# Performance work log

Measured on AMD Instinct MI355X. Metric: run time of the kernel, lower is better.

The kernel has to match this reference:

```python
import jax, jax.numpy as jnp
import numpy as np

V, E, H, L = 10000, 300, 256, 9   # vocab, embed_dim, hidden_dim, num_labels
B, T = 128, 512                   # batch, seq_len


def setup_inputs() -> dict:
    key = jax.random.key(0)
    ks = jax.random.split(key, 14)
    s = 0.05
    emb = jax.random.normal(ks[2], (V, E), jnp.float32) * s
    emb = emb.at[0].set(0.0)  # padding_idx=0
    return {
        "input_ids": jax.random.randint(ks[0], (B, T), 0, V),
        "attention_mask": jnp.ones((B, T), jnp.int32),
        "labels": jax.random.randint(ks[1], (B, T), 0, L),
        "emb": emb,
        "Wih_f": jax.random.normal(ks[3], (4 * H, E), jnp.float32) * s,
        "Whh_f": jax.random.normal(ks[4], (4 * H, H), jnp.float32) * s,
        "b_f": jnp.zeros((4 * H,), jnp.float32),
        "Wih_b": jax.random.normal(ks[5], (4 * H, E), jnp.float32) * s,
        "Whh_b": jax.random.normal(ks[6], (4 * H, H), jnp.float32) * s,
        "b_b": jnp.zeros((4 * H,), jnp.float32),
        "Wc": jax.random.normal(ks[7], (L, 2 * H), jnp.float32) * s,
        "bc": jnp.zeros((L,), jnp.float32),
        "transitions": jax.random.normal(ks[8], (L, L), jnp.float32) * 0.1,
        "start_trans": jax.random.normal(ks[9], (L,), jnp.float32) * 0.1,
        "end_trans": jax.random.normal(ks[10], (L,), jnp.float32) * 0.1,
    }


def _lstm_dir(x, Wih, Whh, b):
    # x: (T, B, E) -> hidden states (T, B, H); PyTorch gate order i,f,g,o
    Bn = x.shape[1]
    h0 = jnp.zeros((Bn, Whh.shape[1]), x.dtype)
    c0 = jnp.zeros((Bn, Whh.shape[1]), x.dtype)
    # precompute input projections once (big GEMM), scan only does small HxH GEMM
    xp = jnp.einsum('tbe,ge->tbg', x, Wih) + b
    def step(carry, xg):
        h, c = carry
        g = xg + h @ Whh.T
        i, f, gg, o = jnp.split(g, 4, axis=-1)
        c = jax.nn.sigmoid(f) * c + jax.nn.sigmoid(i) * jnp.tanh(gg)
        h = jax.nn.sigmoid(o) * jnp.tanh(c)
        return (h, c), h
    _, hs = jax.lax.scan(step, (h0, c0), xp)
    return hs


def reference(input_ids, attention_mask, labels, emb, Wih_f, Whh_f, b_f,
              Wih_b, Whh_b, b_b, Wc, bc, transitions, start_trans, end_trans):
    x = emb[input_ids]                       # (B, T, E)
    xt = jnp.transpose(x, (1, 0, 2))         # (T, B, E)
    hf = _lstm_dir(xt, Wih_f, Whh_f, b_f)
    hb = _lstm_dir(xt[::-1], Wih_b, Whh_b, b_b)[::-1]
    h = jnp.concatenate([hf, hb], axis=-1)   # (T, B, 2H); dropout is identity in eval
    em = h @ Wc.T + bc                       # (T, B, L) emissions

    mask = jnp.transpose(attention_mask, (1, 0)).astype(bool)  # (T, B)
    tags = jnp.transpose(labels, (1, 0))                        # (T, B)
    Bn = em.shape[1]
    bidx = jnp.arange(Bn)

    # --- numerator: score of gold path (torchcrf._compute_score) ---
    score0 = start_trans[tags[0]] + em[0, bidx, tags[0]]
    def num_step(carry, inp):
        score, prev = carry
        e_t, t_t, m_t = inp
        score = score + (transitions[prev, t_t] + e_t[bidx, t_t]) * m_t
        return (score, t_t), None
    (score, _), _ = jax.lax.scan(
        num_step, (score0, tags[0]),
        (em[1:], tags[1:], mask[1:].astype(em.dtype)))
    seq_ends = mask.astype(jnp.int32).sum(0) - 1
    last_tags = tags[seq_ends, bidx]
    score = score + end_trans[last_tags]

    # --- denominator: log partition (torchcrf._compute_normalizer) ---
    alpha0 = start_trans + em[0]             # (B, L)
    def den_step(alpha, inp):
        e_t, m_t = inp
        nxt = jax.nn.logsumexp(alpha[:, :, None] + transitions[None] + e_t[:, None, :], axis=1)
        return jnp.where(m_t[:, None], nxt, alpha), None
    alpha, _ = jax.lax.scan(den_step, alpha0, (em[1:], mask[1:]))
    logZ = jax.nn.logsumexp(alpha + end_trans, axis=-1)

    llh = score - logZ
    return -jnp.mean(llh)  # crf(..., reduction='mean'), negated
```

## Files before the change

kernel.cpp:

```cpp
#include <hip/hip_runtime.h>
#include <hip/hip_bf16.h>
#include <hip/hip_fp16.h>

#define Vn 10000
#define En 300
#define E2n 150
#define Hn 256
#define Gn 1024
#define Ln 9
#define Bn 128
#define Tn 512

#if defined(__has_builtin)
#  if __has_builtin(__builtin_amdgcn_sdot8)
#    define HAS_SDOT8 1
#  endif
#  if __has_builtin(__builtin_amdgcn_fdot2)
#    define HAS_FDOT2 1
#  endif
#endif
#ifndef HAS_SDOT8
#  define HAS_SDOT8 0
#endif
#ifndef HAS_FDOT2
#  define HAS_FDOT2 0
#endif

typedef _Float16 half2_t __attribute__((ext_vector_type(2)));

static __device__ __forceinline__ float bf2f(unsigned short u) {
    return __uint_as_float(((unsigned int)u) << 16);
}
static __device__ __forceinline__ unsigned short f2bf(float f) {
    unsigned int x = __float_as_uint(f);
    return (unsigned short)((x + 0x7FFFu + ((x >> 16) & 1u)) >> 16);
}
static __device__ __forceinline__ float sigm(float x) {
    return 1.f / (1.f + __expf(-x));
}
static __device__ __forceinline__ float tanh_fast(float x) {
    return 2.f / (1.f + __expf(-2.f * x)) - 1.f;
}
static __device__ __forceinline__ int dot8(unsigned int w, int h, int acc) {
#if HAS_SDOT8
    return __builtin_amdgcn_sdot8((int)w, h, acc, false);
#else
    unsigned int wl = ((w & 0x0F0F0F0Fu) ^ 0x08080808u) - 0x08080808u;
    unsigned int wh = (((w >> 4) & 0x0F0F0F0Fu) ^ 0x08080808u) - 0x08080808u;
    unsigned int hl = (((unsigned)h & 0x0F0F0F0Fu) ^ 0x08080808u) - 0x08080808u;
    unsigned int hh = ((((unsigned)h >> 4) & 0x0F0F0F0Fu) ^ 0x08080808u) - 0x08080808u;
    acc = __builtin_amdgcn_sdot4((int)wl, (int)hl, acc, false);
    return __builtin_amdgcn_sdot4((int)wh, (int)hh, acc, false);
#endif
}
static __device__ __forceinline__ float fdot2f(unsigned int a, unsigned int b, float acc) {
#if HAS_FDOT2
    return __builtin_amdgcn_fdot2(__builtin_bit_cast(half2_t, a),
                                  __builtin_bit_cast(half2_t, b), acc, false);
#else
    half2_t av = __builtin_bit_cast(half2_t, a);
    half2_t bv = __builtin_bit_cast(half2_t, b);
    return acc + (float)av.x * (float)bv.x + (float)av.y * (float)bv.y;
#endif
}
static __device__ __forceinline__ unsigned int packf16(float a, float b) {
    half2_t v = {(_Float16)a, (_Float16)b};
    return __builtin_bit_cast(unsigned int, v);
}

__global__ __launch_bounds__(256) void k_prep_emb(
    const float* __restrict__ emb, unsigned int* __restrict__ embp) {
    int n = blockIdx.x * 256 + threadIdx.x;
    if (n >= Vn * E2n) return;
    int v = n / E2n, e2 = n % E2n;
    float a = emb[(size_t)v * En + 2 * e2];
    float b = emb[(size_t)v * En + 2 * e2 + 1];
    embp[n] = packf16(a, b);
}

__global__ __launch_bounds__(256) void k_prep_wt(
    const float* __restrict__ Wf, const float* __restrict__ Wb,
    unsigned int* __restrict__ Tf, unsigned int* __restrict__ Tb) {
    int n = blockIdx.x * 256 + threadIdx.x;
    const float* src = blockIdx.y ? Wb : Wf;
    unsigned int* dst = blockIdx.y ? Tb : Tf;
    int e2 = n / Gn, j = n % Gn;
    float a = src[(size_t)j * En + 2 * e2];
    float b = src[(size_t)j * En + 2 * e2 + 1];
    dst[n] = packf16(a, b);
}

__global__ __launch_bounds__(64) void k_quant_whh(
    const float* __restrict__ Wf, const float* __restrict__ Wb,
    unsigned int* __restrict__ qr_f, unsigned int* __restrict__ ql_f,
    unsigned int* __restrict__ qr_b, unsigned int* __restrict__ ql_b,
    float* __restrict__ scl_f, float* __restrict__ scl_b) {
    int j = blockIdx.x;
    int dir = blockIdx.y;
    int lane = threadIdx.x;
    const float* W = dir ? Wb : Wf;
    float w8[8];
    float m = 0.f;
    if (lane < 32) {
        float4 wlo = *(const float4*)&W[(size_t)j * Hn + 8 * lane];
        float4 whi = *(const float4*)&W[(size_t)j * Hn + 8 * lane + 4];
        w8[0] = wlo.x; w8[1] = wlo.y; w8[2] = wlo.z; w8[3] = wlo.w;
        w8[4] = whi.x; w8[5] = whi.y; w8[6] = whi.z; w8[7] = whi.w;
        #pragma unroll
        for (int i = 0; i < 8; ++i) m = fmaxf(m, fabsf(w8[i]));
    }
    #pragma unroll
    for (int sft = 32; sft >= 1; sft >>= 1) m = fmaxf(m, __shfl_xor(m, sft, 64));
    float inv = (m > 0.f) ? (7.f / m) : 0.f;
    if (lane < 32) {
        unsigned int d = 0;
        #pragma unroll
        for (int i = 0; i < 8; ++i) {
            int qi = (int)rintf(w8[i] * inv);
            d |= ((unsigned int)(qi & 0xF)) << (4 * i);
        }
        if (lane < 24)
            (dir ? qr_b : qr_f)[(size_t)((lane >> 2) * 1024 + j) * 4 + (lane & 3)] = d;
        else {
            int e = lane - 24;
            (dir ? ql_b : ql_f)[(size_t)((e >> 2) * 1024 + j) * 4 + (e & 3)] = d;
        }
    }
    if (lane == 0) (dir ? scl_b : scl_f)[j] = m / 49.f;
}

__global__ __launch_bounds__(256) void k_proj(
    const unsigned int* __restrict__ embp,
    const unsigned int* __restrict__ WT16_f, const unsigned int* __restrict__ WT16_b,
    const float* __restrict__ b_f, const float* __restrict__ b_b,
    unsigned short* __restrict__ Pf, unsigned short* __restrict__ Pb) {
    int tid = threadIdx.x;
    int tx = tid & 63, ty = tid >> 6;
    int dir = blockIdx.z;
    const unsigned int* WT = dir ? WT16_b : WT16_f;
    const float* bias = dir ? b_b : b_f;
    unsigned short* P = dir ? Pb : Pf;
    int v0 = blockIdx.x * 32 + ty * 8;
    int j0 = blockIdx.y * 256 + tx * 4;
    int vr[8];
    #pragma unroll
    for (int r = 0; r < 8; ++r) { int v = v0 + r; vr[r] = (v < Vn) ? v : Vn - 1; }
    float4 acc[8];
    #pragma unroll
    for (int r = 0; r < 8; ++r) acc[r] = make_float4(0.f, 0.f, 0.f, 0.f);
    for (int e2 = 0; e2 < E2n; ++e2) {
        uint4 w = *(const uint4*)&WT[(size_t)e2 * Gn + j0];
        #pragma unroll
        for (int r = 0; r < 8; ++r) {
            unsigned int a = embp[(size_t)vr[r] * E2n + e2];
            acc[r].x = fdot2f(a, w.x, acc[r].x);
            acc[r].y = fdot2f(a, w.y, acc[r].y);
            acc[r].z = fdot2f(a, w.z, acc[r].z);
            acc[r].w = fdot2f(a, w.w, acc[r].w);
        }
    }
    float4 bb = *(const float4*)&bias[j0];
    #pragma unroll
    for (int r = 0; r < 8; ++r) {
        if (v0 + r < Vn) {
            ushort4 o;
            o.x = f2bf(acc[r].x + bb.x); o.y = f2bf(acc[r].y + bb.y);
            o.z = f2bf(acc[r].z + bb.z); o.w = f2bf(acc[r].w + bb.w);
            *(ushort4*)&P[(size_t)(v0 + r) * Gn + j0] = o;
        }
    }
}

__global__ __launch_bounds__(1024, 4) void k_lstm(
    const int* __restrict__ ids,
    const uint4* __restrict__ qr_f, const uint4* __restrict__ ql_f,
    const uint4* __restrict__ qr_b, const uint4* __restrict__ ql_b,
    const float* __restrict__ scl_f, const float* __restrict__ scl_b,
    const unsigned short* __restrict__ Pf, const unsigned short* __restrict__ Pb,
    unsigned short* __restrict__ hs_f, unsigned short* __restrict__ hs_b) {
    __shared__ uint4 wlds[2 * 1024];
    __shared__ float g_stage[Gn];
    __shared__ uint4 h4v[8];
    __shared__ int ids_lds[Tn];
    int tid = threadIdx.x;
    int dir = blockIdx.x >> 7;
    int batch = blockIdx.x & 127;
    const uint4* qr = dir ? qr_b : qr_f;
    const uint4* ql = dir ? ql_b : ql_f;
    const unsigned short* P = dir ? Pb : Pf;
    unsigned short* hs = dir ? hs_b : hs_f;

    unsigned int wReg[24];
    #pragma unroll
    for (int d4 = 0; d4 < 6; ++d4) {
        uint4 v = qr[(size_t)d4 * 1024 + tid];
        wReg[4*d4+0] = v.x; wReg[4*d4+1] = v.y; wReg[4*d4+2] = v.z; wReg[4*d4+3] = v.w;
    }
    wlds[tid] = ql[tid];
    wlds[1024 + tid] = ql[1024 + tid];
    float sc = (dir ? scl_b : scl_f)[tid];
    if (tid < Tn) ids_lds[tid] = ids[batch * Tn + tid];
    if (tid < 8) { uint4 z = {0u, 0u, 0u, 0u}; h4v[tid] = z; }
    float c = 0.f;
    __syncthreads();

    int t0 = dir ? (Tn - 1) : 0;
    float p = bf2f(P[(size_t)ids_lds[t0] * Gn + tid]);

    for (int s = 0; s < Tn; ++s) {
        asm volatile("" : "+v"(wReg[0]), "+v"(wReg[1]), "+v"(wReg[2]), "+v"(wReg[3]),
                          "+v"(wReg[4]), "+v"(wReg[5]), "+v"(wReg[6]), "+v"(wReg[7]),
                          "+v"(wReg[8]), "+v"(wReg[9]), "+v"(wReg[10]), "+v"(wReg[11]));
        asm volatile("" : "+v"(wReg[12]), "+v"(wReg[13]), "+v"(wReg[14]), "+v"(wReg[15]),
                          "+v"(wReg[16]), "+v"(wReg[17]), "+v"(wReg[18]), "+v"(wReg[19]),
                          "+v"(wReg[20]), "+v"(wReg[21]), "+v"(wReg[22]), "+v"(wReg[23]));

        int t = dir ? (Tn - 1 - s) : s;
        int s2 = (s + 1 < Tn) ? s + 1 : Tn - 1;
        int t2 = dir ? (Tn - 1 - s2) : s2;
        unsigned short nx = P[(size_t)ids_lds[t2] * Gn + tid];

        uint4 hq  = h4v[tid & 7];
        uint4 wv0 = wlds[tid];
        uint4 wv1 = wlds[1024 + tid];

        int a0 = 0, a1 = 0, a2 = 0, a3 = 0;
        #pragma unroll
        for (int g = 0; g < 6; ++g) {
            int h0 = __builtin_amdgcn_readlane((int)hq.x, g);
            int h1 = __builtin_amdgcn_readlane((int)hq.y, g);
            int h2 = __builtin_amdgcn_readlane((int)hq.z, g);
            int h3 = __builtin_amdgcn_readlane((int)hq.w, g);
            a0 = dot8(wReg[4*g+0], h0, a0);
            a1 = dot8(wReg[4*g+1], h1, a1);
            a2 = dot8(wReg[4*g+2], h2, a2);
            a3 = dot8(wReg[4*g+3], h3, a3);
        }
        {
            int h0 = __builtin_amdgcn_readlane((int)hq.x, 6);
            int h1 = __builtin_amdgcn_readlane((int)hq.y, 6);
            int h2 = __builtin_amdgcn_readlane((int)hq.z, 6);
            int h3 = __builtin_amdgcn_readlane((int)hq.w, 6);
            a0 = dot8(wv0.x, h0, a0);
            a1 = dot8(wv0.y, h1, a1);
            a2 = dot8(wv0.z, h2, a2);
            a3 = dot8(wv0.w, h3, a3);
            h0 = __builtin_amdgcn_readlane((int)hq.x, 7);
            h1 = __builtin_amdgcn_readlane((int)hq.y, 7);
            h2 = __builtin_amdgcn_readlane((int)hq.z, 7);
            h3 = __builtin_amdgcn_readlane((int)hq.w, 7);
            a0 = dot8(wv1.x, h0, a0);
            a1 = dot8(wv1.y, h1, a1);
            a2 = dot8(wv1.z, h2, a2);
            a3 = dot8(wv1.w, h3, a3);
        }
        g_stage[tid] = sc * (float)((a0 + a1) + (a2 + a3)) + p;
        __syncthreads();
        if (tid < Hn) {
            float gi = g_stage[tid];
            float gf = g_stage[tid + 256];
            float gg = g_stage[tid + 512];
            float go = g_stage[tid + 768];
            float cn = sigm(gf) * c + sigm(gi) * tanh_fast(gg);
            float hn = sigm(go) * tanh_fast(cn);
            c = cn;
            hs[(size_t)(t * Bn + batch) * Hn + tid] = f2bf(hn);
            int qh = (int)rintf(7.f * hn);
            int qo = __shfl_xor(qh, 1, 64);
            if ((tid & 1) == 0)
                ((char*)h4v)[tid >> 1] = (char)((qh & 0xF) | ((qo & 0xF) << 4));
        }
        __syncthreads();
        p = bf2f(nx);
    }
}

__global__ __launch_bounds__(256) void k_emit(
    const unsigned short* __restrict__ hs_f, const unsigned short* __restrict__ hs_b,
    const float* __restrict__ Wc, const float* __restrict__ bc,
    float* __restrict__ em) {
    __shared__ float wc_s[Ln * 2 * Hn];
    int tid = threadIdx.x;
    for (int i = tid; i < Ln * 2 * Hn; i += 256) wc_s[i] = Wc[i];
    __syncthreads();
    int lane = tid & 63, wid = tid >> 6;
    int tb = blockIdx.x * 4 + wid;
    const unsigned short* hf = hs_f + (size_t)tb * Hn;
    const unsigned short* hb = hs_b + (size_t)tb * Hn;
    uint2 uf = *(const uint2*)&hf[lane * 4];
    uint2 ub = *(const uint2*)&hb[lane * 4];
    float f0 = __uint_as_float(uf.x << 16), f1 = __uint_as_float(uf.x & 0xFFFF0000u);
    float f2v = __uint_as_float(uf.y << 16), f3 = __uint_as_float(uf.y & 0xFFFF0000u);
    float b0 = __uint_as_float(ub.x << 16), b1 = __uint_as_float(ub.x & 0xFFFF0000u);
    float b2 = __uint_as_float(ub.y << 16), b3 = __uint_as_float(ub.y & 0xFFFF0000u);
    #pragma unroll
    for (int l = 0; l < Ln; ++l) {
        const float* w = &wc_s[l * 2 * Hn];
        float p = f0 * w[4 * lane] + f1 * w[4 * lane + 1]
                + f2v * w[4 * lane + 2] + f3 * w[4 * lane + 3]
                + b0 * w[Hn + 4 * lane] + b1 * w[Hn + 4 * lane + 1]
                + b2 * w[Hn + 4 * lane + 2] + b3 * w[Hn + 4 * lane + 3];
        #pragma unroll
        for (int m = 32; m >= 1; m >>= 1) p += __shfl_xor(p, m, 64);
        if (lane == 0) em[(size_t)tb * Ln + l] = p + bc[l];
    }
}

__global__ __launch_bounds__(64) void k_crf(
    const float* __restrict__ em, const int* __restrict__ labels,
    const int* __restrict__ mask, const float* __restrict__ trans,
    const float* __restrict__ start, const float* __restrict__ endt,
    float* __restrict__ score, float* __restrict__ logZ) {
    int lane = threadIdx.x;
    int grp = lane >> 5;
    int b = blockIdx.x + 64 * grp;
    int lj = lane & 31;
    int jj = (lj < Ln) ? lj : Ln - 1;
    int base = lane & 32;
    float trj[Ln];
    #pragma unroll
    for (int i = 0; i < Ln; ++i) trj[i] = trans[i * Ln + jj];
    float alpha = start[jj] + em[(size_t)b * Ln + jj];
    float e1 = em[(size_t)(1 * Bn + b) * Ln + jj];
    float e2 = em[(size_t)(2 * Bn + b) * Ln + jj];
    int m1 = mask[b * Tn + 1];
    int m2 = mask[b * Tn + 2];

    float nacc = 0.f; int ncnt = 0;
    bool numlane = (lj >= 16);
    if (numlane) {
        int tq = lj - 16;
        for (int k = 0; k < Tn / 16; ++k) {
            int t = tq + 16 * k;
            int tag = labels[b * Tn + t];
            int mt = mask[b * Tn + t];
            ncnt += mt;
            float e = em[(size_t)(t * Bn + b) * Ln + tag];
            if (t == 0) {
                nacc += start[tag] + e;
            } else {
                int prev = labels[b * Tn + t - 1];
                if (mt) nacc += trans[prev * Ln + tag] + e;
            }
        }
    }

    for (int t = 1; t < Tn; ++t) {
        float s0 = __shfl(alpha, base + 0, 64) + trj[0];
        float s1 = __shfl(alpha, base + 1, 64) + trj[1];
        float s2 = __shfl(alpha, base + 2, 64) + trj[2];
        float s3 = __shfl(alpha, base + 3, 64) + trj[3];
        float s4 = __shfl(alpha, base + 4, 64) + trj[4];
        float s5 = __shfl(alpha, base + 5, 64) + trj[5];
        float s6 = __shfl(alpha, base + 6, 64) + trj[6];
        float s7 = __shfl(alpha, base + 7, 64) + trj[7];
        float s8 = __shfl(alpha, base + 8, 64) + trj[8];
        float mx = fmaxf(fmaxf(fmaxf(s0, s1), fmaxf(s2, s3)),
                         fmaxf(fmaxf(s4, s5), fmaxf(fmaxf(s6, s7), s8)));
        float sum = __expf(s0 - mx) + __expf(s1 - mx) + __expf(s2 - mx)
                  + __expf(s3 - mx) + __expf(s4 - mx) + __expf(s5 - mx)
                  + __expf(s6 - mx) + __expf(s7 - mx) + __expf(s8 - mx);
        float nxt = mx + __logf(sum) + e1;
        if (m1) alpha = nxt;
        e1 = e2; m1 = m2;
        int t2 = (t + 2 < Tn) ? t + 2 : Tn - 1;
        e2 = em[(size_t)(t2 * Bn + b) * Ln + jj];
        m2 = mask[b * Tn + t2];
    }
    float s = (lj < Ln) ? alpha + endt[lj] : -1e30f;
    float mx = s;
    #pragma unroll
    for (int d = 16; d >= 1; d >>= 1) mx = fmaxf(mx, __shfl_xor(mx, d, 64));
    float sm = __expf(s - mx);
    #pragma unroll
    for (int d = 16; d >= 1; d >>= 1) sm += __shfl_xor(sm, d, 64);
    if (lj == 0) logZ[b] = mx + __logf(sm);
    if (!numlane) { nacc = 0.f; ncnt = 0; }
    #pragma unroll
    for (int d = 8; d >= 1; d >>= 1) {
        nacc += __shfl_xor(nacc, d, 64);
        ncnt += __shfl_xor(ncnt, d, 64);
    }
    if (lj == 16) {
        int send = ncnt - 1;
        int last = labels[b * Tn + send];
        score[b] = nacc + endt[last];
    }
}

__global__ __launch_bounds__(128) void k_final(
    const float* __restrict__ score, const float* __restrict__ logZ,
    float* __restrict__ out) {
    __shared__ float s_s[128];
    int tid = threadIdx.x;
    s_s[tid] = score[tid] - logZ[tid];
    #pragma unroll
    for (int m = 64; m >= 1; m >>= 1) {
        __syncthreads();
        if (tid < m) s_s[tid] += s_s[tid + m];
    }
    if (tid == 0) out[0] = -s_s[0] / (float)Bn;
}

extern "C" void kernel_launch(void* const* d_in, const int* in_sizes, int n_in,
                              void* d_out, int out_size, void* d_ws, size_t ws_size,
                              hipStream_t stream) {
    const int* ids = (const int*)d_in[0];
    const int* msk = (const int*)d_in[1];
    const int* lbl = (const int*)d_in[2];
    const float* emb = (const float*)d_in[3];
    const float* Wih_f = (const float*)d_in[4];
    const float* Whh_f = (const float*)d_in[5];
    const float* b_f = (const float*)d_in[6];
    const float* Wih_b = (const float*)d_in[7];
    const float* Whh_b = (const float*)d_in[8];
    const float* b_b = (const float*)d_in[9];
    const float* Wc = (const float*)d_in[10];
    const float* bc = (const float*)d_in[11];
    const float* trans = (const float*)d_in[12];
    const float* st = (const float*)d_in[13];
    const float* en = (const float*)d_in[14];

    char* ws = (char*)d_ws;
    unsigned int* WT16_f = (unsigned int*)ws;   ws += (size_t)E2n * Gn * 4;
    unsigned int* WT16_b = (unsigned int*)ws;   ws += (size_t)E2n * Gn * 4;
    unsigned int* qr_f = (unsigned int*)ws;     ws += 98304;
    unsigned int* ql_f = (unsigned int*)ws;     ws += 32768;
    unsigned int* qr_b = (unsigned int*)ws;     ws += 98304;
    unsigned int* ql_b = (unsigned int*)ws;     ws += 32768;
    float* scl_f = (float*)ws;                  ws += 4096;
    float* scl_b = (float*)ws;                  ws += 4096;
    unsigned short* Pf = (unsigned short*)ws;   ws += (size_t)Vn * Gn * 2;
    unsigned short* Pb = (unsigned short*)ws;   ws += (size_t)Vn * Gn * 2;
    unsigned short* hs_f = (unsigned short*)ws; ws += (size_t)Tn * Bn * Hn * 2;
    unsigned short* hs_b = (unsigned short*)ws; ws += (size_t)Tn * Bn * Hn * 2;
    float* em = (float*)ws;                     ws += (size_t)Tn * Bn * Ln * 4;
    float* score = (float*)ws;                  ws += 512;
    float* logZ = (float*)ws;                   ws += 512;
    unsigned int* embp = (unsigned int*)hs_f;

    k_prep_emb<<<(Vn * E2n + 255) / 256, 256, 0, stream>>>(emb, embp);
    k_prep_wt<<<dim3((E2n * Gn) / 256, 2), 256, 0, stream>>>(Wih_f, Wih_b, WT16_f, WT16_b);
    k_quant_whh<<<dim3(1024, 2), 64, 0, stream>>>(Whh_f, Whh_b, qr_f, ql_f, qr_b, ql_b, scl_f, scl_b);
    k_proj<<<dim3(313, 4, 2), 256, 0, stream>>>(embp, WT16_f, WT16_b, b_f, b_b, Pf, Pb);
    k_lstm<<<256, 1024, 0, stream>>>(ids,
        (const uint4*)qr_f, (const uint4*)ql_f, (const uint4*)qr_b, (const uint4*)ql_b,
        scl_f, scl_b, Pf, Pb, hs_f, hs_b);
    k_emit<<<16384, 256, 0, stream>>>(hs_f, hs_b, Wc, bc, em);
    k_crf<<<64, 64, 0, stream>>>(em, lbl, msk, trans, st, en, score, logZ);
    k_final<<<1, 128, 0, stream>>>(score, logZ, (float*)d_out);
}
```

Measured before the change: 947.5 us.

## Fuse prep kernels, use packed fp16 FMA in projection, batch emit, split CRF numerator

```diff
diff --git a/kernel.cpp b/kernel.cpp
--- a/kernel.cpp
+++ b/kernel.cpp
@@ -15,15 +15,9 @@
 #  if __has_builtin(__builtin_amdgcn_sdot8)
 #    define HAS_SDOT8 1
 #  endif
-#  if __has_builtin(__builtin_amdgcn_fdot2)
-#    define HAS_FDOT2 1
-#  endif
 #endif
 #ifndef HAS_SDOT8
 #  define HAS_SDOT8 0
-#endif
-#ifndef HAS_FDOT2
-#  define HAS_FDOT2 0
 #endif
 
 typedef _Float16 half2_t __attribute__((ext_vector_type(2)));
@@ -53,52 +47,52 @@
     return __builtin_amdgcn_sdot4((int)wh, (int)hh, acc, false);
 #endif
 }
-static __device__ __forceinline__ float fdot2f(unsigned int a, unsigned int b, float acc) {
-#if HAS_FDOT2
-    return __builtin_amdgcn_fdot2(__builtin_bit_cast(half2_t, a),
-                                  __builtin_bit_cast(half2_t, b), acc, false);
-#else
-    half2_t av = __builtin_bit_cast(half2_t, a);
-    half2_t bv = __builtin_bit_cast(half2_t, b);
-    return acc + (float)av.x * (float)bv.x + (float)av.y * (float)bv.y;
-#endif
-}
 static __device__ __forceinline__ unsigned int packf16(float a, float b) {
     half2_t v = {(_Float16)a, (_Float16)b};
     return __builtin_bit_cast(unsigned int, v);
 }
-
-__global__ __launch_bounds__(256) void k_prep_emb(
-    const float* __restrict__ emb, unsigned int* __restrict__ embp) {
-    int n = blockIdx.x * 256 + threadIdx.x;
-    if (n >= Vn * E2n) return;
-    int v = n / E2n, e2 = n % E2n;
-    float a = emb[(size_t)v * En + 2 * e2];
-    float b = emb[(size_t)v * En + 2 * e2 + 1];
-    embp[n] = packf16(a, b);
-}
-
-__global__ __launch_bounds__(256) void k_prep_wt(
-    const float* __restrict__ Wf, const float* __restrict__ Wb,
-    unsigned int* __restrict__ Tf, unsigned int* __restrict__ Tb) {
-    int n = blockIdx.x * 256 + threadIdx.x;
-    const float* src = blockIdx.y ? Wb : Wf;
-    unsigned int* dst = blockIdx.y ? Tb : Tf;
-    int e2 = n / Gn, j = n % Gn;
-    float a = src[(size_t)j * En + 2 * e2];
-    float b = src[(size_t)j * En + 2 * e2 + 1];
-    dst[n] = packf16(a, b);
-}
-
-__global__ __launch_bounds__(64) void k_quant_whh(
-    const float* __restrict__ Wf, const float* __restrict__ Wb,
+static __device__ __forceinline__ half2_t h2(unsigned int u) {
+    return __builtin_bit_cast(half2_t, u);
+}
+
+#define NPREP_A 5860
+#define NPREP_B 1200
+#define NPREP_C 512
+
+__global__ __launch_bounds__(256) void k_prep(
+    const float* __restrict__ emb, unsigned int* __restrict__ embp,
+    const float* __restrict__ Wih_f, const float* __restrict__ Wih_b,
+    unsigned int* __restrict__ WT16_f, unsigned int* __restrict__ WT16_b,
+    const float* __restrict__ Whh_f, const float* __restrict__ Whh_b,
     unsigned int* __restrict__ qr_f, unsigned int* __restrict__ ql_f,
     unsigned int* __restrict__ qr_b, unsigned int* __restrict__ ql_b,
     float* __restrict__ scl_f, float* __restrict__ scl_b) {
-    int j = blockIdx.x;
-    int dir = blockIdx.y;
-    int lane = threadIdx.x;
-    const float* W = dir ? Wb : Wf;
+    int bx = blockIdx.x, tid = threadIdx.x;
+    if (bx < NPREP_A) {
+        int n = bx * 256 + tid;
+        if (n < Vn * E2n) {
+            int v = n / E2n, e2 = n % E2n;
+            embp[n] = packf16(emb[(size_t)v * En + 2 * e2],
+                              emb[(size_t)v * En + 2 * e2 + 1]);
+        }
+        return;
+    }
+    if (bx < NPREP_A + NPREP_B) {
+        int m = (bx - NPREP_A) * 256 + tid;
+        int dir = m / 153600;
+        int n = m % 153600;
+        const float* src = dir ? Wih_b : Wih_f;
+        unsigned int* dst = dir ? WT16_b : WT16_f;
+        int e2 = n / Gn, j = n % Gn;
+        dst[n] = packf16(src[(size_t)j * En + 2 * e2],
+                         src[(size_t)j * En + 2 * e2 + 1]);
+        return;
+    }
+    int idx = (bx - NPREP_A - NPREP_B) * 4 + (tid >> 6);
+    int dir = idx >> 10;
+    int j = idx & 1023;
+    int lane = tid & 63;
+    const float* W = dir ? Whh_b : Whh_f;
     float w8[8];
     float m = 0.f;
     if (lane < 32) {
@@ -145,18 +139,23 @@
     int vr[8];
     #pragma unroll
     for (int r = 0; r < 8; ++r) { int v = v0 + r; vr[r] = (v < Vn) ? v : Vn - 1; }
-    float4 acc[8];
-    #pragma unroll
-    for (int r = 0; r < 8; ++r) acc[r] = make_float4(0.f, 0.f, 0.f, 0.f);
-    for (int e2 = 0; e2 < E2n; ++e2) {
-        uint4 w = *(const uint4*)&WT[(size_t)e2 * Gn + j0];
+    half2_t ax[8], ay[8], az[8], aw[8];
+    #pragma unroll
+    for (int r = 0; r < 8; ++r) {
+        half2_t z = {(_Float16)0.f, (_Float16)0.f};
+        ax[r] = z; ay[r] = z; az[r] = z; aw[r] = z;
+    }
+    for (int e2 = 0; e2 < E2n; e2 += 2) {
+        uint4 w0 = *(const uint4*)&WT[(size_t)(e2 + 0) * Gn + j0];
+        uint4 w1 = *(const uint4*)&WT[(size_t)(e2 + 1) * Gn + j0];
         #pragma unroll
         for (int r = 0; r < 8; ++r) {
-            unsigned int a = embp[(size_t)vr[r] * E2n + e2];
-            acc[r].x = fdot2f(a, w.x, acc[r].x);
-            acc[r].y = fdot2f(a, w.y, acc[r].y);
-            acc[r].z = fdot2f(a, w.z, acc[r].z);
-            acc[r].w = fdot2f(a, w.w, acc[r].w);
+            uint2 a = *(const uint2*)&embp[(size_t)vr[r] * E2n + e2];
+            half2_t a0 = h2(a.x), a1 = h2(a.y);
+            ax[r] += a0 * h2(w0.x); ay[r] += a0 * h2(w0.y);
+            az[r] += a0 * h2(w0.z); aw[r] += a0 * h2(w0.w);
+            ax[r] += a1 * h2(w1.x); ay[r] += a1 * h2(w1.y);
+            az[r] += a1 * h2(w1.z); aw[r] += a1 * h2(w1.w);
         }
     }
     float4 bb = *(const float4*)&bias[j0];
@@ -164,8 +163,10 @@
     for (int r = 0; r < 8; ++r) {
         if (v0 + r < Vn) {
             ushort4 o;
-            o.x = f2bf(acc[r].x + bb.x); o.y = f2bf(acc[r].y + bb.y);
-            o.z = f2bf(acc[r].z + bb.z); o.w = f2bf(acc[r].w + bb.w);
+            o.x = f2bf((float)ax[r].x + (float)ax[r].y + bb.x);
+            o.y = f2bf((float)ay[r].x + (float)ay[r].y + bb.y);
+            o.z = f2bf((float)az[r].x + (float)az[r].y + bb.z);
+            o.w = f2bf((float)aw[r].x + (float)aw[r].y + bb.w);
             *(ushort4*)&P[(size_t)(v0 + r) * Gn + j0] = o;
         }
     }
@@ -229,29 +230,29 @@
         for (int g = 0; g < 6; ++g) {
             int h0 = __builtin_amdgcn_readlane((int)hq.x, g);
             int h1 = __builtin_amdgcn_readlane((int)hq.y, g);
-            int h2 = __builtin_amdgcn_readlane((int)hq.z, g);
+            int h2v = __builtin_amdgcn_readlane((int)hq.z, g);
             int h3 = __builtin_amdgcn_readlane((int)hq.w, g);
             a0 = dot8(wReg[4*g+0], h0, a0);
             a1 = dot8(wReg[4*g+1], h1, a1);
-            a2 = dot8(wReg[4*g+2], h2, a2);
+            a2 = dot8(wReg[4*g+2], h2v, a2);
             a3 = dot8(wReg[4*g+3], h3, a3);
         }
         {
             int h0 = __builtin_amdgcn_readlane((int)hq.x, 6);
             int h1 = __builtin_amdgcn_readlane((int)hq.y, 6);
-            int h2 = __builtin_amdgcn_readlane((int)hq.z, 6);
+            int h2v = __builtin_amdgcn_readlane((int)hq.z, 6);
             int h3 = __builtin_amdgcn_readlane((int)hq.w, 6);
             a0 = dot8(wv0.x, h0, a0);
             a1 = dot8(wv0.y, h1, a1);
-            a2 = dot8(wv0.z, h2, a2);
+            a2 = dot8(wv0.z, h2v, a2);
             a3 = dot8(wv0.w, h3, a3);
             h0 = __builtin_amdgcn_readlane((int)hq.x, 7);
             h1 = __builtin_amdgcn_readlane((int)hq.y, 7);
-            h2 = __builtin_amdgcn_readlane((int)hq.z, 7);
+            h2v = __builtin_amdgcn_readlane((int)hq.z, 7);
             h3 = __builtin_amdgcn_readlane((int)hq.w, 7);
             a0 = dot8(wv1.x, h0, a0);
             a1 = dot8(wv1.y, h1, a1);
-            a2 = dot8(wv1.z, h2, a2);
+            a2 = dot8(wv1.z, h2v, a2);
             a3 = dot8(wv1.w, h3, a3);
         }
         g_stage[tid] = sc * (float)((a0 + a1) + (a2 + a3)) + p;
@@ -284,25 +285,28 @@
     for (int i = tid; i < Ln * 2 * Hn; i += 256) wc_s[i] = Wc[i];
     __syncthreads();
     int lane = tid & 63, wid = tid >> 6;
-    int tb = blockIdx.x * 4 + wid;
-    const unsigned short* hf = hs_f + (size_t)tb * Hn;
-    const unsigned short* hb = hs_b + (size_t)tb * Hn;
-    uint2 uf = *(const uint2*)&hf[lane * 4];
-    uint2 ub = *(const uint2*)&hb[lane * 4];
-    float f0 = __uint_as_float(uf.x << 16), f1 = __uint_as_float(uf.x & 0xFFFF0000u);
-    float f2v = __uint_as_float(uf.y << 16), f3 = __uint_as_float(uf.y & 0xFFFF0000u);
-    float b0 = __uint_as_float(ub.x << 16), b1 = __uint_as_float(ub.x & 0xFFFF0000u);
-    float b2 = __uint_as_float(ub.y << 16), b3 = __uint_as_float(ub.y & 0xFFFF0000u);
-    #pragma unroll
-    for (int l = 0; l < Ln; ++l) {
-        const float* w = &wc_s[l * 2 * Hn];
-        float p = f0 * w[4 * lane] + f1 * w[4 * lane + 1]
-                + f2v * w[4 * lane + 2] + f3 * w[4 * lane + 3]
-                + b0 * w[Hn + 4 * lane] + b1 * w[Hn + 4 * lane + 1]
-                + b2 * w[Hn + 4 * lane + 2] + b3 * w[Hn + 4 * lane + 3];
-        #pragma unroll
-        for (int m = 32; m >= 1; m >>= 1) p += __shfl_xor(p, m, 64);
-        if (lane == 0) em[(size_t)tb * Ln + l] = p + bc[l];
+    int tb0 = blockIdx.x * 16 + wid * 4;
+    for (int i = 0; i < 4; ++i) {
+        int tb = tb0 + i;
+        const unsigned short* hf = hs_f + (size_t)tb * Hn;
+        const unsigned short* hb = hs_b + (size_t)tb * Hn;
+        uint2 uf = *(const uint2*)&hf[lane * 4];
+        uint2 ub = *(const uint2*)&hb[lane * 4];
+        float f0 = __uint_as_float(uf.x << 16), f1 = __uint_as_float(uf.x & 0xFFFF0000u);
+        float f2v = __uint_as_float(uf.y << 16), f3 = __uint_as_float(uf.y & 0xFFFF0000u);
+        float b0 = __uint_as_float(ub.x << 16), b1 = __uint_as_float(ub.x & 0xFFFF0000u);
+        float b2 = __uint_as_float(ub.y << 16), b3 = __uint_as_float(ub.y & 0xFFFF0000u);
+        #pragma unroll
+        for (int l = 0; l < Ln; ++l) {
+            const float* w = &wc_s[l * 2 * Hn];
+            float pe = f0 * w[4 * lane] + f1 * w[4 * lane + 1]
+                     + f2v * w[4 * lane + 2] + f3 * w[4 * lane + 3]
+                     + b0 * w[Hn + 4 * lane] + b1 * w[Hn + 4 * lane + 1]
+                     + b2 * w[Hn + 4 * lane + 2] + b3 * w[Hn + 4 * lane + 3];
+            #pragma unroll
+            for (int m = 32; m >= 1; m >>= 1) pe += __shfl_xor(pe, m, 64);
+            if (lane == 0) em[(size_t)tb * Ln + l] = pe + bc[l];
+        }
     }
 }
 
@@ -312,6 +316,33 @@
     const float* __restrict__ start, const float* __restrict__ endt,
     float* __restrict__ score, float* __restrict__ logZ) {
     int lane = threadIdx.x;
+    if (blockIdx.x >= 64) {
+        int b = blockIdx.x - 64;
+        float acc = 0.f; int cnt = 0;
+        for (int t = lane; t < Tn; t += 64) {
+            int tag = labels[b * Tn + t];
+            int mt = mask[b * Tn + t];
+            cnt += mt;
+            float e = em[(size_t)(t * Bn + b) * Ln + tag];
+            if (t == 0) {
+                acc += start[tag] + e;
+            } else {
+                int prev = labels[b * Tn + t - 1];
+                if (mt) acc += trans[prev * Ln + tag] + e;
+            }
+        }
+        #pragma unroll
+        for (int m = 32; m >= 1; m >>= 1) {
+            acc += __shfl_xor(acc, m, 64);
+            cnt += __shfl_xor(cnt, m, 64);
+        }
+        if (lane == 0) {
+            int send = cnt - 1;
+            int last = labels[b * Tn + send];
+            score[b] = acc + endt[last];
+        }
+        return;
+    }
     int grp = lane >> 5;
     int b = blockIdx.x + 64 * grp;
     int lj = lane & 31;
@@ -325,26 +356,6 @@
     float e2 = em[(size_t)(2 * Bn + b) * Ln + jj];
     int m1 = mask[b * Tn + 1];
     int m2 = mask[b * Tn + 2];
-
-    float nacc = 0.f; int ncnt = 0;
-    bool numlane = (lj >= 16);
-    if (numlane) {
-        int tq = lj - 16;
-        for (int k = 0; k < Tn / 16; ++k) {
-            int t = tq + 16 * k;
-            int tag = labels[b * Tn + t];
-            int mt = mask[b * Tn + t];
-            ncnt += mt;
-            float e = em[(size_t)(t * Bn + b) * Ln + tag];
-            if (t == 0) {
-                nacc += start[tag] + e;
-            } else {
-                int prev = labels[b * Tn + t - 1];
-                if (mt) nacc += trans[prev * Ln + tag] + e;
-            }
-        }
-    }
-
     for (int t = 1; t < Tn; ++t) {
         float s0 = __shfl(alpha, base + 0, 64) + trj[0];
         float s1 = __shfl(alpha, base + 1, 64) + trj[1];
@@ -375,17 +386,6 @@
     #pragma unroll
     for (int d = 16; d >= 1; d >>= 1) sm += __shfl_xor(sm, d, 64);
     if (lj == 0) logZ[b] = mx + __logf(sm);
-    if (!numlane) { nacc = 0.f; ncnt = 0; }
-    #pragma unroll
-    for (int d = 8; d >= 1; d >>= 1) {
-        nacc += __shfl_xor(nacc, d, 64);
-        ncnt += __shfl_xor(ncnt, d, 64);
-    }
-    if (lj == 16) {
-        int send = ncnt - 1;
-        int last = labels[b * Tn + send];
-        score[b] = nacc + endt[last];
-    }
 }
 
 __global__ __launch_bounds__(128) void k_final(
@@ -439,14 +439,14 @@
     float* logZ = (float*)ws;                   ws += 512;
     unsigned int* embp = (unsigned int*)hs_f;
 
-    k_prep_emb<<<(Vn * E2n + 255) / 256, 256, 0, stream>>>(emb, embp);
-    k_prep_wt<<<dim3((E2n * Gn) / 256, 2), 256, 0, stream>>>(Wih_f, Wih_b, WT16_f, WT16_b);
-    k_quant_whh<<<dim3(1024, 2), 64, 0, stream>>>(Whh_f, Whh_b, qr_f, ql_f, qr_b, ql_b, scl_f, scl_b);
+    k_prep<<<NPREP_A + NPREP_B + NPREP_C, 256, 0, stream>>>(
+        emb, embp, Wih_f, Wih_b, WT16_f, WT16_b,
+        Whh_f, Whh_b, qr_f, ql_f, qr_b, ql_b, scl_f, scl_b);
     k_proj<<<dim3(313, 4, 2), 256, 0, stream>>>(embp, WT16_f, WT16_b, b_f, b_b, Pf, Pb);
     k_lstm<<<256, 1024, 0, stream>>>(ids,
         (const uint4*)qr_f, (const uint4*)ql_f, (const uint4*)qr_b, (const uint4*)ql_b,
         scl_f, scl_b, Pf, Pb, hs_f, hs_b);
-    k_emit<<<16384, 256, 0, stream>>>(hs_f, hs_b, Wc, bc, em);
-    k_crf<<<64, 64, 0, stream>>>(em, lbl, msk, trans, st, en, score, logZ);
+    k_emit<<<4096, 256, 0, stream>>>(hs_f, hs_b, Wc, bc, em);
+    k_crf<<<192, 64, 0, stream>>>(em, lbl, msk, trans, st, en, score, logZ);
     k_final<<<1, 128, 0, stream>>>(score, logZ, (float*)d_out);
 }
```

Result: faster. 909.3 us, median of 2 (-4.0%).
